# Optimization experiments

Hardware: AMD Instinct MI355X
Metric: run time of the kernel (lower is better)

## Reference

```python
import jax, jax.numpy as jnp
import numpy as np

B, S, H, T, F, L = 32, 512, 1024, 100, 512, 5  # batch, seq, hidden, num_topics, topic_hidden, n_langs
EPS = 1e-5


def _layernorm(x, g, b):
    mu = jnp.mean(x, axis=-1, keepdims=True)
    var = jnp.mean((x - mu) ** 2, axis=-1, keepdims=True)
    return (x - mu) * jax.lax.rsqrt(var + EPS) * g + b


def setup_inputs() -> dict:
    key = jax.random.key(0)
    ks = jax.random.split(key, 16)
    sc = 0.02
    return {
        "sequence_output": jax.random.normal(ks[0], (B, S, H), dtype=jnp.float32),
        "attention_mask": jnp.ones((B, S), dtype=jnp.float32),
        "language_ids": jax.random.randint(ks[1], (B,), 0, L, dtype=jnp.int32),
        "lda_features": jax.random.uniform(ks[2], (B, T), dtype=jnp.float32),
        # per-language adapter params (stacked over L)
        "W1": jax.random.normal(ks[3], (L, H, H), dtype=jnp.float32) * sc,
        "b1": jnp.zeros((L, H), dtype=jnp.float32),
        "g1": jnp.ones((L, H), dtype=jnp.float32),
        "beta1": jnp.zeros((L, H), dtype=jnp.float32),
        "W2": jax.random.normal(ks[4], (L, H, H), dtype=jnp.float32) * sc,
        "b2": jnp.zeros((L, H), dtype=jnp.float32),
        # topic fusion params
        "Wf": jax.random.normal(ks[5], (H + T, F), dtype=jnp.float32) * sc,
        "bf": jnp.zeros((F,), dtype=jnp.float32),
        "gf": jnp.ones((F,), dtype=jnp.float32),
        "betaf": jnp.zeros((F,), dtype=jnp.float32),
    }


def reference(sequence_output, attention_mask, language_ids, lda_features,
              W1, b1, g1, beta1, W2, b2, Wf, bf, gf, betaf):
    # Apply every language adapter to the full batch, then mask-accumulate
    # (faithful to the original anti-pattern).
    adapted = jnp.zeros_like(sequence_output)
    for lang in range(L):
        h = jnp.einsum("bsh,he->bse", sequence_output, W1[lang]) + b1[lang]
        h = jax.nn.relu(_layernorm(h, g1[lang], beta1[lang]))
        h = jnp.einsum("bsh,he->bse", h, W2[lang]) + b2[lang]
        lang_mask = (language_ids == lang).astype(sequence_output.dtype)[:, None, None]
        adapted = adapted + lang_mask * h
    # masked mean pool over sequence
    masked = adapted * attention_mask[:, :, None]
    pooled = masked.sum(axis=1) / attention_mask.sum(axis=1)[:, None]  # [B, H]
    combined = jnp.concatenate([pooled, lda_features], axis=-1)        # [B, H+T]
    fused = _layernorm(combined @ Wf + bf, gf, betaf)
    return jax.nn.relu(fused)  # dropout is identity in eval
```

## Files before the change

### kernel.cpp

```cpp
#include <hip/hip_runtime.h>
#include <hip/hip_bf16.h>
#include <stdint.h>

#define Bq 32
#define Sq 512
#define Hq 1024
#define Tq 100
#define Fq 512
#define Lq 5
#define EPSq 1e-5f

typedef float fx4 __attribute__((ext_vector_type(4)));
typedef __bf16 bfx8 __attribute__((ext_vector_type(8)));
typedef unsigned short u16x8 __attribute__((ext_vector_type(8)));

static __device__ __forceinline__ unsigned short f2bf(float f) {
  unsigned int u = __builtin_bit_cast(unsigned int, f);
  return (unsigned short)((u + 0x7fffu + ((u >> 16) & 1u)) >> 16);
}
static __device__ __forceinline__ float bf2f(unsigned short s) {
  return __builtin_bit_cast(float, ((unsigned int)s) << 16);
}
static __device__ __forceinline__ u16x8 cvt8(float4 x0, float4 x1) {
  u16x8 r;
  r[0] = f2bf(x0.x); r[1] = f2bf(x0.y); r[2] = f2bf(x0.z); r[3] = f2bf(x0.w);
  r[4] = f2bf(x1.x); r[5] = f2bf(x1.y); r[6] = f2bf(x1.z); r[7] = f2bf(x1.w);
  return r;
}
static __device__ __forceinline__ void gl_lds16(const void* g, void* l) {
  __builtin_amdgcn_global_load_lds(
      (const __attribute__((address_space(1))) unsigned int*)(uintptr_t)g,
      (__attribute__((address_space(3))) unsigned int*)(uintptr_t)l,
      16, 0, 0);
}

__global__ void k_prep(const float* __restrict__ w1, unsigned short* __restrict__ w1t) {
  __shared__ float t[32][33];
  int blk = blockIdx.x;
  int l = blk >> 10; int rem = blk & 1023; int tr = rem >> 5; int tc = rem & 31;
  const float* src = w1 + (size_t)l * Hq * Hq;
  unsigned short* dst = w1t + (size_t)l * Hq * Hq;
  int tid = threadIdx.x;
  int tx = tid & 31, ty = tid >> 5;
#pragma unroll
  for (int p = 0; p < 4; p++)
    t[ty + 8 * p][tx] = src[(size_t)(tr * 32 + ty + 8 * p) * Hq + tc * 32 + tx];
  __syncthreads();
#pragma unroll
  for (int p = 0; p < 4; p++)
    dst[(size_t)(tc * 32 + ty + 8 * p) * Hq + tr * 32 + tx] = f2bf(t[tx][ty + 8 * p]);
}

#define HS_ITER(HS, C0A, C0B, C1A, C1B, N0A, N0B, N1A, N1B)                          \
  do {                                                                               \
    int cur = (HS) & 3;                                                              \
    if ((HS) < 30)                                                                   \
      asm volatile("s_waitcnt vmcnt(8) lgkmcnt(0)\n\ts_barrier" ::: "memory");       \
    else                                                                             \
      asm volatile("s_waitcnt vmcnt(0) lgkmcnt(0)\n\ts_barrier" ::: "memory");       \
    if ((HS) <= 28) {                                                                \
      int ko = ((HS) + 3) * 32;                                                      \
      N0A = *(const float4*)(gAf0 + ko); N0B = *(const float4*)(gAf0 + ko + 4);      \
      N1A = *(const float4*)(gAf1 + ko); N1B = *(const float4*)(gAf1 + ko + 4);      \
      int slot = ((HS) + 3) & 3;                                                     \
      gl_lds16(gB[0] + ko, (char*)sB[slot] + dstOff[0]);                             \
      gl_lds16(gB[1] + ko, (char*)sB[slot] + dstOff[1]);                             \
    }                                                                                \
    const char* cA = (const char*)sA[cur];                                           \
    const char* cB = (const char*)sB[cur];                                           \
    bfx8 bfr[4], af[8];                                                              \
    _Pragma("unroll") for (int n = 0; n < 4; n++)                                    \
        bfr[n] = *(const bfx8*)(cB + bOff[n]);                                       \
    _Pragma("unroll") for (int m = 0; m < 8; m++)                                    \
        af[m] = *(const bfx8*)(cA + aOff[m]);                                        \
    __builtin_amdgcn_s_setprio(1);                                                   \
    _Pragma("unroll") for (int m = 0; m < 8; m++)                                    \
      _Pragma("unroll") for (int n = 0; n < 4; n++)                                  \
          acc[m][n] = __builtin_amdgcn_mfma_f32_16x16x32_bf16(af[m], bfr[n],         \
                                                              acc[m][n], 0, 0, 0);  \
    __builtin_amdgcn_s_setprio(0);                                                   \
    if ((HS) <= 29) {                                                                \
      int sa = ((HS) + 2) & 3;                                                       \
      *(u16x8*)((char*)sA[sa] + aW0) = cvt8(C0A, C0B);                               \
      *(u16x8*)((char*)sA[sa] + aW1) = cvt8(C1A, C1B);                               \
    }                                                                                \
  } while (0)

__global__ __launch_bounds__(512, 2) void k_gemm1(const float* __restrict__ seq,
                                                  const unsigned short* __restrict__ w1t,
                                                  const float* __restrict__ b1,
                                                  const int* __restrict__ lid,
                                                  unsigned short* __restrict__ h1bf) {
  __shared__ short sA[4][256 * 32];
  __shared__ short sB[4][256 * 32];
  int bid = blockIdx.x;
  int g = bid & 63; int tn = bid >> 6;
  int b = g >> 1; int tm = g & 1;
  int lang = lid[b];
  const float* Abf = seq + (size_t)b * Sq * Hq + (size_t)tm * 256 * Hq;
  const unsigned short* Bb = w1t + (size_t)lang * Hq * Hq + (size_t)tn * 256 * Hq;

  int tid = threadIdx.x;
  int lane = tid & 63; int wid = tid >> 6;
  int wr = wid >> 2, wc = wid & 3;
  int fr = lane & 15;
  int q = lane >> 4;
  int key = ((fr >> 1) & 7) << 4;

  const float* gAf0; const float* gAf1; int aW0, aW1;
  {
    int c0 = tid;       int R0 = c0 >> 2, q0 = c0 & 3; int y0 = R0 * 64 + q0 * 16;
    int c1 = tid + 512; int R1 = c1 >> 2, q1 = c1 & 3; int y1 = R1 * 64 + q1 * 16;
    aW0 = y0 ^ ((y0 >> 3) & 0x70);
    aW1 = y1 ^ ((y1 >> 3) & 0x70);
    gAf0 = Abf + (size_t)R0 * Hq + q0 * 8;
    gAf1 = Abf + (size_t)R1 * Hq + q1 * 8;
  }
  const unsigned short* gB[2]; int dstOff[2];
#pragma unroll
  for (int j = 0; j < 2; j++) {
    int p = (tid + j * 512) * 16;
    int l = p ^ ((p >> 3) & 0x70);
    int R = l >> 6, qa = (l >> 4) & 3;
    gB[j] = Bb + (size_t)R * Hq + qa * 8;
    dstOff[j] = p;
  }

  int aOff[8], bOff[4];
#pragma unroll
  for (int m = 0; m < 8; m++)
    aOff[m] = ((wr * 128 + m * 16 + fr) * 64 + q * 16) ^ key;
#pragma unroll
  for (int n = 0; n < 4; n++)
    bOff[n] = ((wc * 64 + n * 16 + fr) * 64 + q * 16) ^ key;

  fx4 acc[8][4];
#pragma unroll
  for (int m = 0; m < 8; m++)
#pragma unroll
    for (int n = 0; n < 4; n++) acc[m][n] = (fx4){0.f, 0.f, 0.f, 0.f};

  {
    float4 t0a = *(const float4*)(gAf0);      float4 t0b = *(const float4*)(gAf0 + 4);
    float4 t1a = *(const float4*)(gAf1);      float4 t1b = *(const float4*)(gAf1 + 4);
    *(u16x8*)((char*)sA[0] + aW0) = cvt8(t0a, t0b);
    *(u16x8*)((char*)sA[0] + aW1) = cvt8(t1a, t1b);
    t0a = *(const float4*)(gAf0 + 32); t0b = *(const float4*)(gAf0 + 36);
    t1a = *(const float4*)(gAf1 + 32); t1b = *(const float4*)(gAf1 + 36);
    *(u16x8*)((char*)sA[1] + aW0) = cvt8(t0a, t0b);
    *(u16x8*)((char*)sA[1] + aW1) = cvt8(t1a, t1b);
  }
  gl_lds16(gB[0],      (char*)sB[0] + dstOff[0]);
  gl_lds16(gB[1],      (char*)sB[0] + dstOff[1]);
  gl_lds16(gB[0] + 32, (char*)sB[1] + dstOff[0]);
  gl_lds16(gB[1] + 32, (char*)sB[1] + dstOff[1]);
  float4 x0a, x0b, x1a, x1b, y0a, y0b, y1a, y1b;
  x0a = *(const float4*)(gAf0 + 64); x0b = *(const float4*)(gAf0 + 68);
  x1a = *(const float4*)(gAf1 + 64); x1b = *(const float4*)(gAf1 + 68);
  gl_lds16(gB[0] + 64, (char*)sB[2] + dstOff[0]);
  gl_lds16(gB[1] + 64, (char*)sB[2] + dstOff[1]);

  for (int hs = 0; hs < 32; hs += 2) {
    HS_ITER(hs,     x0a, x0b, x1a, x1b, y0a, y0b, y1a, y1b);
    HS_ITER(hs + 1, y0a, y0b, y1a, y1b, x0a, x0b, x1a, x1b);
  }

  unsigned short* Cb = h1bf + (size_t)b * Sq * Hq;
  float bv[4];
#pragma unroll
  for (int n = 0; n < 4; n++)
    bv[n] = b1[lang * Hq + tn * 256 + wc * 64 + n * 16 + fr];
  int r0 = q * 4;
#pragma unroll
  for (int m = 0; m < 8; m++) {
#pragma unroll
    for (int n = 0; n < 4; n++) {
      int col = tn * 256 + wc * 64 + n * 16 + fr;
#pragma unroll
      for (int r = 0; r < 4; r++) {
        int row = tm * 256 + wr * 128 + m * 16 + r0 + r;
        Cb[(size_t)row * Hq + col] = f2bf(acc[m][n][r] + bv[n]);
      }
    }
  }
}

__global__ __launch_bounds__(256) void k_ln_pool(const unsigned short* __restrict__ h1bf,
                                                 const float* __restrict__ g1,
                                                 const float* __restrict__ be1,
                                                 const float* __restrict__ mask,
                                                 const int* __restrict__ lid,
                                                 float* __restrict__ partial) {
  __shared__ float sacc[4][1024];
  int blk = blockIdx.x; int b = blk >> 3; int ch = blk & 7;
  int tid = threadIdx.x; int lane = tid & 63; int w = tid >> 6;
  int lang = lid[b];
  int e0 = lane * 8;
  int e1 = 512 + lane * 8;

  const float4* gp = (const float4*)(g1 + (size_t)lang * Hq);
  const float4* bp = (const float4*)(be1 + (size_t)lang * Hq);
  float4 ga0 = gp[lane * 2], ga1 = gp[lane * 2 + 1];
  float4 gb0 = gp[128 + lane * 2], gb1 = gp[129 + lane * 2];
  float4 ba0 = bp[lane * 2], ba1 = bp[lane * 2 + 1];
  float4 bb0 = bp[128 + lane * 2], bb1 = bp[129 + lane * 2];
  float gA[8] = {ga0.x, ga0.y, ga0.z, ga0.w, ga1.x, ga1.y, ga1.z, ga1.w};
  float gB[8] = {gb0.x, gb0.y, gb0.z, gb0.w, gb1.x, gb1.y, gb1.z, gb1.w};
  float bA[8] = {ba0.x, ba0.y, ba0.z, ba0.w, ba1.x, ba1.y, ba1.z, ba1.w};
  float bB[8] = {bb0.x, bb0.y, bb0.z, bb0.w, bb1.x, bb1.y, bb1.z, bb1.w};

  float acc0[8] = {0, 0, 0, 0, 0, 0, 0, 0}, acc1[8] = {0, 0, 0, 0, 0, 0, 0, 0};

  for (int i = 0; i < 16; i++) {
    int s = ch * 64 + w * 16 + i;
    const unsigned short* rowp = h1bf + ((size_t)b * Sq + s) * Hq;
    u16x8 va = *(const u16x8*)(rowp + e0);
    u16x8 vb = *(const u16x8*)(rowp + e1);
    float xa[8], xb[8];
    float sum = 0.f, sq = 0.f;
#pragma unroll
    for (int j = 0; j < 8; j++) {
      xa[j] = bf2f(va[j]); sum += xa[j]; sq += xa[j] * xa[j];
      xb[j] = bf2f(vb[j]); sum += xb[j]; sq += xb[j] * xb[j];
    }
#pragma unroll
    for (int off = 1; off < 64; off <<= 1) {
      sum += __shfl_xor(sum, off, 64);
      sq += __shfl_xor(sq, off, 64);
    }
    float mu = sum * (1.f / Hq);
    float var = sq * (1.f / Hq) - mu * mu;
    float rstd = rsqrtf(var + EPSq);
    float mw = mask[b * Sq + s];
#pragma unroll
    for (int j = 0; j < 8; j++) {
      float y0 = fmaxf((xa[j] - mu) * rstd * gA[j] + bA[j], 0.f);
      float y1 = fmaxf((xb[j] - mu) * rstd * gB[j] + bB[j], 0.f);
      acc0[j] += mw * y0;
      acc1[j] += mw * y1;
    }
  }
#pragma unroll
  for (int j = 0; j < 8; j++) {
    sacc[w][e0 + j] = acc0[j];
    sacc[w][e1 + j] = acc1[j];
  }
  __syncthreads();
  int e = tid * 4;
#pragma unroll
  for (int j = 0; j < 4; j++)
    partial[(size_t)blk * Hq + e + j] =
        sacc[0][e + j] + sacc[1][e + j] + sacc[2][e + j] + sacc[3][e + j];
}

__global__ __launch_bounds__(256) void k_gemm2p(const float* __restrict__ partial,
                                                const float* __restrict__ mask,
                                                const float* __restrict__ w2,
                                                const int* __restrict__ lid,
                                                float* __restrict__ g2part) {
  __shared__ float pl[256];
  __shared__ float wsum[4];
  int blk = blockIdx.x;
  int b = blk >> 3; int ch = (blk >> 2) & 1; int ks = blk & 3;
  int tid = threadIdx.x;
  int lang = lid[b];
  float mv = mask[b * Sq + tid] + mask[b * Sq + 256 + tid];
#pragma unroll
  for (int off = 1; off < 64; off <<= 1) mv += __shfl_xor(mv, off, 64);
  if ((tid & 63) == 0) wsum[tid >> 6] = mv;
  __syncthreads();
  float inv = 1.0f / (wsum[0] + wsum[1] + wsum[2] + wsum[3]);
  float s = 0.f;
#pragma unroll
  for (int c = 0; c < 8; c++) s += partial[((size_t)(b * 8 + c)) * Hq + ks * 256 + tid];
  pl[tid] = s * inv;
  __syncthreads();
  int col = ch * 512 + tid * 2;
  const float* W = w2 + (size_t)lang * Hq * Hq + (size_t)ks * 256 * Hq + col;
  float a0 = 0.f, a1 = 0.f;
  for (int e0 = 0; e0 < 256; e0 += 8) {
    float2 w[8];
#pragma unroll
    for (int j = 0; j < 8; j++) w[j] = *(const float2*)(W + (size_t)(e0 + j) * Hq);
#pragma unroll
    for (int j = 0; j < 8; j++) { float c = pl[e0 + j]; a0 += c * w[j].x; a1 += c * w[j].y; }
  }
  float2* dst = (float2*)(g2part + ((size_t)(b * 4 + ks) * Hq) + col);
  *dst = make_float2(a0, a1);
}

__global__ __launch_bounds__(256) void k_fpart(const float* __restrict__ g2part,
                                               const float* __restrict__ b2,
                                               const int* __restrict__ lid,
                                               const float* __restrict__ lda,
                                               const float* __restrict__ wf,
                                               float* __restrict__ fpart) {
  __shared__ float sc[128];
  int blk = blockIdx.x;
  int b = blk / 9, ks = blk % 9;
  int tid = threadIdx.x;
  int klen = (ks < 8) ? 128 : 100;
  int kbase = (ks < 8) ? ks * 128 : Hq;
  if (ks < 8) {
    if (tid < 128) {
      int col = kbase + tid;
      float v = b2[lid[b] * Hq + col];
#pragma unroll
      for (int c = 0; c < 4; c++) v += g2part[((size_t)(b * 4 + c)) * Hq + col];
      sc[tid] = v;
    }
  } else if (tid < 100) {
    sc[tid] = lda[b * Tq + tid];
  }
  __syncthreads();
  const float* W = wf + (size_t)kbase * Fq + tid * 2;
  float a0 = 0.f, a1 = 0.f;
  int k0 = 0;
  for (; k0 + 8 <= klen; k0 += 8) {
    float2 w[8];
#pragma unroll
    for (int j = 0; j < 8; j++) w[j] = *(const float2*)(W + (size_t)(k0 + j) * Fq);
#pragma unroll
    for (int j = 0; j < 8; j++) { float c = sc[k0 + j]; a0 += c * w[j].x; a1 += c * w[j].y; }
  }
  for (; k0 < klen; k0++) {
    float2 w = *(const float2*)(W + (size_t)k0 * Fq);
    float c = sc[k0];
    a0 += c * w.x; a1 += c * w.y;
  }
  float2* dst = (float2*)(fpart + (size_t)blk * Fq + tid * 2);
  *dst = make_float2(a0, a1);
}

__global__ __launch_bounds__(512) void k_final2(const float* __restrict__ fpart,
                                                const float* __restrict__ bff,
                                                const float* __restrict__ gf,
                                                const float* __restrict__ betaf,
                                                float* __restrict__ out) {
  __shared__ float rsum[8], rsq[8];
  int b = blockIdx.x; int tid = threadIdx.x;
  float acc = bff[tid];
#pragma unroll
  for (int ks = 0; ks < 9; ks++) acc += fpart[((size_t)b * 9 + ks) * Fq + tid];
  float s = acc, q = acc * acc;
#pragma unroll
  for (int off = 1; off < 64; off <<= 1) {
    s += __shfl_xor(s, off, 64);
    q += __shfl_xor(q, off, 64);
  }
  int w = tid >> 6, lane = tid & 63;
  if (lane == 0) { rsum[w] = s; rsq[w] = q; }
  __syncthreads();
  float S = 0.f, Q = 0.f;
#pragma unroll
  for (int i = 0; i < 8; i++) { S += rsum[i]; Q += rsq[i]; }
  float mu = S * (1.f / Fq);
  float var = Q * (1.f / Fq) - mu * mu;
  float y = (acc - mu) * rsqrtf(var + EPSq) * gf[tid] + betaf[tid];
  y = fmaxf(y, 0.f);
  out[b * Fq + tid] = y;
}

extern "C" void kernel_launch(void* const* d_in, const int* in_sizes, int n_in,
                              void* d_out, int out_size, void* d_ws, size_t ws_size,
                              hipStream_t stream) {
  const float* seq = (const float*)d_in[0];
  const float* mask = (const float*)d_in[1];
  const int* lid = (const int*)d_in[2];
  const float* lda = (const float*)d_in[3];
  const float* W1 = (const float*)d_in[4];
  const float* b1 = (const float*)d_in[5];
  const float* g1 = (const float*)d_in[6];
  const float* be1 = (const float*)d_in[7];
  const float* W2 = (const float*)d_in[8];
  const float* b2 = (const float*)d_in[9];
  const float* Wf = (const float*)d_in[10];
  const float* bff = (const float*)d_in[11];
  const float* gf = (const float*)d_in[12];
  const float* betaf = (const float*)d_in[13];
  float* out = (float*)d_out;

  char* ws = (char*)d_ws;
  unsigned short* w1t = (unsigned short*)(ws);
  unsigned short* h1bf = (unsigned short*)(ws + 10485760);
  float* partial = (float*)(ws + 44040192);
  float* g2part = (float*)(ws + 45088768);
  float* fpart = (float*)(ws + 45613056);

  k_prep<<<5120, 256, 0, stream>>>(W1, w1t);
  k_gemm1<<<256, 512, 0, stream>>>(seq, w1t, b1, lid, h1bf);
  k_ln_pool<<<256, 256, 0, stream>>>(h1bf, g1, be1, mask, lid, partial);
  k_gemm2p<<<256, 256, 0, stream>>>(partial, mask, W2, lid, g2part);
  k_fpart<<<288, 256, 0, stream>>>(g2part, b2, lid, lda, Wf, fpart);
  k_final2<<<32, 512, 0, stream>>>(fpart, bff, gf, betaf, out);
}
```

Measured before the change: 91.36 us.

## Fuse LayerNorm, ReLU and masked pooling into GEMM1 with full-row tiles

```diff
diff --git a/kernel.cpp b/kernel.cpp
--- a/kernel.cpp
+++ b/kernel.cpp
@@ -13,18 +13,15 @@
 typedef float fx4 __attribute__((ext_vector_type(4)));
 typedef __bf16 bfx8 __attribute__((ext_vector_type(8)));
 typedef unsigned short u16x8 __attribute__((ext_vector_type(8)));
+typedef unsigned short u16x4 __attribute__((ext_vector_type(4)));
 
 static __device__ __forceinline__ unsigned short f2bf(float f) {
   unsigned int u = __builtin_bit_cast(unsigned int, f);
   return (unsigned short)((u + 0x7fffu + ((u >> 16) & 1u)) >> 16);
 }
-static __device__ __forceinline__ float bf2f(unsigned short s) {
-  return __builtin_bit_cast(float, ((unsigned int)s) << 16);
-}
-static __device__ __forceinline__ u16x8 cvt8(float4 x0, float4 x1) {
-  u16x8 r;
-  r[0] = f2bf(x0.x); r[1] = f2bf(x0.y); r[2] = f2bf(x0.z); r[3] = f2bf(x0.w);
-  r[4] = f2bf(x1.x); r[5] = f2bf(x1.y); r[6] = f2bf(x1.z); r[7] = f2bf(x1.w);
+static __device__ __forceinline__ u16x4 cvt4(float4 x) {
+  u16x4 r;
+  r[0] = f2bf(x.x); r[1] = f2bf(x.y); r[2] = f2bf(x.z); r[3] = f2bf(x.w);
   return r;
 }
 static __device__ __forceinline__ void gl_lds16(const void* g, void* l) {
@@ -51,206 +48,185 @@
     dst[(size_t)(tc * 32 + ty + 8 * p) * Hq + tr * 32 + tx] = f2bf(t[tx][ty + 8 * p]);
 }
 
-#define HS_ITER(HS, C0A, C0B, C1A, C1B, N0A, N0B, N1A, N1B)                          \
+#define HS_ITER(HS, CUR, NXT)                                                        \
   do {                                                                               \
-    int cur = (HS) & 3;                                                              \
-    if ((HS) < 30)                                                                   \
-      asm volatile("s_waitcnt vmcnt(8) lgkmcnt(0)\n\ts_barrier" ::: "memory");       \
+    int cur = (HS) & 1;                                                              \
+    if ((HS) < 31)                                                                   \
+      asm volatile("s_waitcnt vmcnt(1) lgkmcnt(0)\n\ts_barrier" ::: "memory");       \
     else                                                                             \
       asm volatile("s_waitcnt vmcnt(0) lgkmcnt(0)\n\ts_barrier" ::: "memory");       \
-    if ((HS) <= 28) {                                                                \
-      int ko = ((HS) + 3) * 32;                                                      \
-      N0A = *(const float4*)(gAf0 + ko); N0B = *(const float4*)(gAf0 + ko + 4);      \
-      N1A = *(const float4*)(gAf1 + ko); N1B = *(const float4*)(gAf1 + ko + 4);      \
-      int slot = ((HS) + 3) & 3;                                                     \
-      gl_lds16(gB[0] + ko, (char*)sB[slot] + dstOff[0]);                             \
-      gl_lds16(gB[1] + ko, (char*)sB[slot] + dstOff[1]);                             \
+    if ((HS) <= 30) {                                                                \
+      int ko = ((HS) + 1) * 32;                                                      \
+      int sl = ((HS) + 1) & 1;                                                       \
+      _Pragma("unroll") for (int j = 0; j < 8; j++)                                  \
+          gl_lds16(gBsrc[j] + ko, (char*)sB[sl] + pB[j]);                            \
+    }                                                                                \
+    if ((HS) <= 29) {                                                                \
+      NXT = *(const float4*)(gAsrc + ((HS) + 2) * 32);                               \
     }                                                                                \
     const char* cA = (const char*)sA[cur];                                           \
     const char* cB = (const char*)sB[cur];                                           \
-    bfx8 bfr[4], af[8];                                                              \
-    _Pragma("unroll") for (int n = 0; n < 4; n++)                                    \
+    bfx8 af[4], bfr[8];                                                              \
+    _Pragma("unroll") for (int m = 0; m < 4; m++)                                    \
+        af[m] = *(const bfx8*)(cA + aOff[m]);                                        \
+    _Pragma("unroll") for (int n = 0; n < 8; n++)                                    \
         bfr[n] = *(const bfx8*)(cB + bOff[n]);                                       \
-    _Pragma("unroll") for (int m = 0; m < 8; m++)                                    \
-        af[m] = *(const bfx8*)(cA + aOff[m]);                                        \
     __builtin_amdgcn_s_setprio(1);                                                   \
-    _Pragma("unroll") for (int m = 0; m < 8; m++)                                    \
-      _Pragma("unroll") for (int n = 0; n < 4; n++)                                  \
+    _Pragma("unroll") for (int m = 0; m < 4; m++)                                    \
+      _Pragma("unroll") for (int n = 0; n < 8; n++)                                  \
           acc[m][n] = __builtin_amdgcn_mfma_f32_16x16x32_bf16(af[m], bfr[n],         \
                                                               acc[m][n], 0, 0, 0);  \
     __builtin_amdgcn_s_setprio(0);                                                   \
-    if ((HS) <= 29) {                                                                \
-      int sa = ((HS) + 2) & 3;                                                       \
-      *(u16x8*)((char*)sA[sa] + aW0) = cvt8(C0A, C0B);                               \
-      *(u16x8*)((char*)sA[sa] + aW1) = cvt8(C1A, C1B);                               \
+    if ((HS) <= 30) {                                                                \
+      int sl = ((HS) + 1) & 1;                                                       \
+      *(u16x4*)((char*)sA[sl] + aW) = cvt4(CUR);                                     \
     }                                                                                \
   } while (0)
 
-__global__ __launch_bounds__(512, 2) void k_gemm1(const float* __restrict__ seq,
-                                                  const unsigned short* __restrict__ w1t,
-                                                  const float* __restrict__ b1,
-                                                  const int* __restrict__ lid,
-                                                  unsigned short* __restrict__ h1bf) {
-  __shared__ short sA[4][256 * 32];
-  __shared__ short sB[4][256 * 32];
+__global__ __launch_bounds__(512, 2) void k_gemm1f(const float* __restrict__ seq,
+                                                   const unsigned short* __restrict__ w1t,
+                                                   const float* __restrict__ b1,
+                                                   const float* __restrict__ g1,
+                                                   const float* __restrict__ be1,
+                                                   const float* __restrict__ mask,
+                                                   const int* __restrict__ lid,
+                                                   float* __restrict__ partial) {
+  __shared__ short sA[2][64 * 32];
+  __shared__ short sB[2][1024 * 32];
   int bid = blockIdx.x;
-  int g = bid & 63; int tn = bid >> 6;
-  int b = g >> 1; int tm = g & 1;
+  int x = bid & 7; int t = bid >> 3; int mblk = t & 7; int b = ((t >> 3) << 3) | x;
   int lang = lid[b];
-  const float* Abf = seq + (size_t)b * Sq * Hq + (size_t)tm * 256 * Hq;
-  const unsigned short* Bb = w1t + (size_t)lang * Hq * Hq + (size_t)tn * 256 * Hq;
+  const float* Abf = seq + ((size_t)b * Sq + (size_t)mblk * 64) * Hq;
+  const unsigned short* Bb = w1t + (size_t)lang * Hq * Hq;
 
   int tid = threadIdx.x;
-  int lane = tid & 63; int wid = tid >> 6;
-  int wr = wid >> 2, wc = wid & 3;
+  int lane = tid & 63; int w = tid >> 6;
   int fr = lane & 15;
   int q = lane >> 4;
   int key = ((fr >> 1) & 7) << 4;
 
-  const float* gAf0; const float* gAf1; int aW0, aW1;
-  {
-    int c0 = tid;       int R0 = c0 >> 2, q0 = c0 & 3; int y0 = R0 * 64 + q0 * 16;
-    int c1 = tid + 512; int R1 = c1 >> 2, q1 = c1 & 3; int y1 = R1 * 64 + q1 * 16;
-    aW0 = y0 ^ ((y0 >> 3) & 0x70);
-    aW1 = y1 ^ ((y1 >> 3) & 0x70);
-    gAf0 = Abf + (size_t)R0 * Hq + q0 * 8;
-    gAf1 = Abf + (size_t)R1 * Hq + q1 * 8;
-  }
-  const unsigned short* gB[2]; int dstOff[2];
-#pragma unroll
-  for (int j = 0; j < 2; j++) {
+  int R = tid >> 3, q8 = tid & 7;
+  int yA = R * 64 + q8 * 8;
+  int aW = yA ^ ((yA >> 3) & 0x70);
+  const float* gAsrc = Abf + (size_t)R * Hq + q8 * 4;
+  const unsigned short* gBsrc[8]; int pB[8];
+#pragma unroll
+  for (int j = 0; j < 8; j++) {
     int p = (tid + j * 512) * 16;
     int l = p ^ ((p >> 3) & 0x70);
-    int R = l >> 6, qa = (l >> 4) & 3;
-    gB[j] = Bb + (size_t)R * Hq + qa * 8;
-    dstOff[j] = p;
-  }
-
-  int aOff[8], bOff[4];
-#pragma unroll
-  for (int m = 0; m < 8; m++)
-    aOff[m] = ((wr * 128 + m * 16 + fr) * 64 + q * 16) ^ key;
-#pragma unroll
-  for (int n = 0; n < 4; n++)
-    bOff[n] = ((wc * 64 + n * 16 + fr) * 64 + q * 16) ^ key;
-
-  fx4 acc[8][4];
-#pragma unroll
-  for (int m = 0; m < 8; m++)
-#pragma unroll
-    for (int n = 0; n < 4; n++) acc[m][n] = (fx4){0.f, 0.f, 0.f, 0.f};
+    gBsrc[j] = Bb + (size_t)(l >> 6) * Hq + ((l >> 4) & 3) * 8;
+    pB[j] = p;
+  }
+  int aOff[4], bOff[8];
+#pragma unroll
+  for (int m = 0; m < 4; m++) aOff[m] = ((m * 16 + fr) * 64 + q * 16) ^ key;
+#pragma unroll
+  for (int n = 0; n < 8; n++) bOff[n] = ((w * 128 + n * 16 + fr) * 64 + q * 16) ^ key;
+
+  fx4 acc[4][8];
+#pragma unroll
+  for (int m = 0; m < 4; m++)
+#pragma unroll
+    for (int n = 0; n < 8; n++) acc[m][n] = (fx4){0.f, 0.f, 0.f, 0.f};
 
   {
-    float4 t0a = *(const float4*)(gAf0);      float4 t0b = *(const float4*)(gAf0 + 4);
-    float4 t1a = *(const float4*)(gAf1);      float4 t1b = *(const float4*)(gAf1 + 4);
-    *(u16x8*)((char*)sA[0] + aW0) = cvt8(t0a, t0b);
-    *(u16x8*)((char*)sA[0] + aW1) = cvt8(t1a, t1b);
-    t0a = *(const float4*)(gAf0 + 32); t0b = *(const float4*)(gAf0 + 36);
-    t1a = *(const float4*)(gAf1 + 32); t1b = *(const float4*)(gAf1 + 36);
-    *(u16x8*)((char*)sA[1] + aW0) = cvt8(t0a, t0b);
-    *(u16x8*)((char*)sA[1] + aW1) = cvt8(t1a, t1b);
-  }
-  gl_lds16(gB[0],      (char*)sB[0] + dstOff[0]);
-  gl_lds16(gB[1],      (char*)sB[0] + dstOff[1]);
-  gl_lds16(gB[0] + 32, (char*)sB[1] + dstOff[0]);
-  gl_lds16(gB[1] + 32, (char*)sB[1] + dstOff[1]);
-  float4 x0a, x0b, x1a, x1b, y0a, y0b, y1a, y1b;
-  x0a = *(const float4*)(gAf0 + 64); x0b = *(const float4*)(gAf0 + 68);
-  x1a = *(const float4*)(gAf1 + 64); x1b = *(const float4*)(gAf1 + 68);
-  gl_lds16(gB[0] + 64, (char*)sB[2] + dstOff[0]);
-  gl_lds16(gB[1] + 64, (char*)sB[2] + dstOff[1]);
+    float4 a0 = *(const float4*)(gAsrc);
+    *(u16x4*)((char*)sA[0] + aW) = cvt4(a0);
+  }
+#pragma unroll
+  for (int j = 0; j < 8; j++) gl_lds16(gBsrc[j], (char*)sB[0] + pB[j]);
+  float4 rcur, rnxt;
+  rcur = *(const float4*)(gAsrc + 32);
 
   for (int hs = 0; hs < 32; hs += 2) {
-    HS_ITER(hs,     x0a, x0b, x1a, x1b, y0a, y0b, y1a, y1b);
-    HS_ITER(hs + 1, y0a, y0b, y1a, y1b, x0a, x0b, x1a, x1b);
-  }
-
-  unsigned short* Cb = h1bf + (size_t)b * Sq * Hq;
-  float bv[4];
-#pragma unroll
-  for (int n = 0; n < 4; n++)
-    bv[n] = b1[lang * Hq + tn * 256 + wc * 64 + n * 16 + fr];
-  int r0 = q * 4;
-#pragma unroll
-  for (int m = 0; m < 8; m++) {
-#pragma unroll
-    for (int n = 0; n < 4; n++) {
-      int col = tn * 256 + wc * 64 + n * 16 + fr;
+    HS_ITER(hs, rcur, rnxt);
+    HS_ITER(hs + 1, rnxt, rcur);
+  }
+
+  __syncthreads();
+  float* red = (float*)sA;
+  float* stats = red + 1024;
+
+  float bv[8], gv[8], bev[8];
+#pragma unroll
+  for (int n = 0; n < 8; n++) {
+    int col = w * 128 + n * 16 + fr;
+    bv[n] = b1[lang * Hq + col];
+    gv[n] = g1[lang * Hq + col];
+    bev[n] = be1[lang * Hq + col];
+  }
+  float rs[4][4], rq[4][4];
+#pragma unroll
+  for (int m = 0; m < 4; m++)
+#pragma unroll
+    for (int r = 0; r < 4; r++) {
+      float s = 0.f, qq = 0.f;
+#pragma unroll
+      for (int n = 0; n < 8; n++) {
+        float v = acc[m][n][r] + bv[n];
+        s += v; qq += v * v;
+      }
+      rs[m][r] = s; rq[m][r] = qq;
+    }
+#pragma unroll
+  for (int off = 1; off < 16; off <<= 1)
+#pragma unroll
+    for (int m = 0; m < 4; m++)
 #pragma unroll
       for (int r = 0; r < 4; r++) {
-        int row = tm * 256 + wr * 128 + m * 16 + r0 + r;
-        Cb[(size_t)row * Hq + col] = f2bf(acc[m][n][r] + bv[n]);
+        rs[m][r] += __shfl_xor(rs[m][r], off, 64);
+        rq[m][r] += __shfl_xor(rq[m][r], off, 64);
+      }
+  if (fr == 0) {
+#pragma unroll
+    for (int m = 0; m < 4; m++)
+#pragma unroll
+      for (int r = 0; r < 4; r++) {
+        int row = m * 16 + q * 4 + r;
+        red[(w * 64 + row) * 2] = rs[m][r];
+        red[(w * 64 + row) * 2 + 1] = rq[m][r];
+      }
+  }
+  __syncthreads();
+  if (tid < 64) {
+    int row = tid;
+    float S = 0.f, Q = 0.f;
+#pragma unroll
+    for (int w8 = 0; w8 < 8; w8++) {
+      S += red[(w8 * 64 + row) * 2];
+      Q += red[(w8 * 64 + row) * 2 + 1];
+    }
+    float mu = S * (1.f / Hq);
+    float var = Q * (1.f / Hq) - mu * mu;
+    stats[row * 3] = mu;
+    stats[row * 3 + 1] = rsqrtf(var + EPSq);
+    stats[row * 3 + 2] = mask[b * Sq + mblk * 64 + row];
+  }
+  __syncthreads();
+  float pol[8] = {0.f, 0.f, 0.f, 0.f, 0.f, 0.f, 0.f, 0.f};
+#pragma unroll
+  for (int m = 0; m < 4; m++)
+#pragma unroll
+    for (int r = 0; r < 4; r++) {
+      int row = m * 16 + q * 4 + r;
+      float mu = stats[row * 3], rstd = stats[row * 3 + 1], mw = stats[row * 3 + 2];
+#pragma unroll
+      for (int n = 0; n < 8; n++) {
+        float v = acc[m][n][r] + bv[n];
+        float y = (v - mu) * rstd * gv[n] + bev[n];
+        pol[n] += mw * fmaxf(y, 0.f);
       }
     }
-  }
-}
-
-__global__ __launch_bounds__(256) void k_ln_pool(const unsigned short* __restrict__ h1bf,
-                                                 const float* __restrict__ g1,
-                                                 const float* __restrict__ be1,
-                                                 const float* __restrict__ mask,
-                                                 const int* __restrict__ lid,
-                                                 float* __restrict__ partial) {
-  __shared__ float sacc[4][1024];
-  int blk = blockIdx.x; int b = blk >> 3; int ch = blk & 7;
-  int tid = threadIdx.x; int lane = tid & 63; int w = tid >> 6;
-  int lang = lid[b];
-  int e0 = lane * 8;
-  int e1 = 512 + lane * 8;
-
-  const float4* gp = (const float4*)(g1 + (size_t)lang * Hq);
-  const float4* bp = (const float4*)(be1 + (size_t)lang * Hq);
-  float4 ga0 = gp[lane * 2], ga1 = gp[lane * 2 + 1];
-  float4 gb0 = gp[128 + lane * 2], gb1 = gp[129 + lane * 2];
-  float4 ba0 = bp[lane * 2], ba1 = bp[lane * 2 + 1];
-  float4 bb0 = bp[128 + lane * 2], bb1 = bp[129 + lane * 2];
-  float gA[8] = {ga0.x, ga0.y, ga0.z, ga0.w, ga1.x, ga1.y, ga1.z, ga1.w};
-  float gB[8] = {gb0.x, gb0.y, gb0.z, gb0.w, gb1.x, gb1.y, gb1.z, gb1.w};
-  float bA[8] = {ba0.x, ba0.y, ba0.z, ba0.w, ba1.x, ba1.y, ba1.z, ba1.w};
-  float bB[8] = {bb0.x, bb0.y, bb0.z, bb0.w, bb1.x, bb1.y, bb1.z, bb1.w};
-
-  float acc0[8] = {0, 0, 0, 0, 0, 0, 0, 0}, acc1[8] = {0, 0, 0, 0, 0, 0, 0, 0};
-
-  for (int i = 0; i < 16; i++) {
-    int s = ch * 64 + w * 16 + i;
-    const unsigned short* rowp = h1bf + ((size_t)b * Sq + s) * Hq;
-    u16x8 va = *(const u16x8*)(rowp + e0);
-    u16x8 vb = *(const u16x8*)(rowp + e1);
-    float xa[8], xb[8];
-    float sum = 0.f, sq = 0.f;
-#pragma unroll
-    for (int j = 0; j < 8; j++) {
-      xa[j] = bf2f(va[j]); sum += xa[j]; sq += xa[j] * xa[j];
-      xb[j] = bf2f(vb[j]); sum += xb[j]; sq += xb[j] * xb[j];
-    }
-#pragma unroll
-    for (int off = 1; off < 64; off <<= 1) {
-      sum += __shfl_xor(sum, off, 64);
-      sq += __shfl_xor(sq, off, 64);
-    }
-    float mu = sum * (1.f / Hq);
-    float var = sq * (1.f / Hq) - mu * mu;
-    float rstd = rsqrtf(var + EPSq);
-    float mw = mask[b * Sq + s];
-#pragma unroll
-    for (int j = 0; j < 8; j++) {
-      float y0 = fmaxf((xa[j] - mu) * rstd * gA[j] + bA[j], 0.f);
-      float y1 = fmaxf((xb[j] - mu) * rstd * gB[j] + bB[j], 0.f);
-      acc0[j] += mw * y0;
-      acc1[j] += mw * y1;
-    }
-  }
-#pragma unroll
-  for (int j = 0; j < 8; j++) {
-    sacc[w][e0 + j] = acc0[j];
-    sacc[w][e1 + j] = acc1[j];
-  }
-  __syncthreads();
-  int e = tid * 4;
-#pragma unroll
-  for (int j = 0; j < 4; j++)
-    partial[(size_t)blk * Hq + e + j] =
-        sacc[0][e + j] + sacc[1][e + j] + sacc[2][e + j] + sacc[3][e + j];
+#pragma unroll
+  for (int n = 0; n < 8; n++) {
+    pol[n] += __shfl_xor(pol[n], 16, 64);
+    pol[n] += __shfl_xor(pol[n], 32, 64);
+  }
+  if (q == 0) {
+#pragma unroll
+    for (int n = 0; n < 8; n++)
+      partial[((size_t)(b * 8 + mblk)) * Hq + w * 128 + n * 16 + fr] = pol[n];
+  }
 }
 
 __global__ __launch_bounds__(256) void k_gemm2p(const float* __restrict__ partial,
@@ -382,14 +358,12 @@
 
   char* ws = (char*)d_ws;
   unsigned short* w1t = (unsigned short*)(ws);
-  unsigned short* h1bf = (unsigned short*)(ws + 10485760);
-  float* partial = (float*)(ws + 44040192);
-  float* g2part = (float*)(ws + 45088768);
-  float* fpart = (float*)(ws + 45613056);
+  float* partial = (float*)(ws + 10485760);
+  float* g2part = (float*)(ws + 11534336);
+  float* fpart = (float*)(ws + 12058624);
 
   k_prep<<<5120, 256, 0, stream>>>(W1, w1t);
-  k_gemm1<<<256, 512, 0, stream>>>(seq, w1t, b1, lid, h1bf);
-  k_ln_pool<<<256, 256, 0, stream>>>(h1bf, g1, be1, mask, lid, partial);
+  k_gemm1f<<<256, 512, 0, stream>>>(seq, w1t, b1, g1, be1, mask, lid, partial);
   k_gemm2p<<<256, 256, 0, stream>>>(partial, mask, W2, lid, g2part);
   k_fpart<<<288, 256, 0, stream>>>(g2part, b2, lid, lda, Wf, fpart);
   k_final2<<<32, 512, 0, stream>>>(fpart, bff, gf, betaf, out);
```

After: 111.9 us. +22.5%, slower.
